# Kernel optimization log

Measured on AMD Instinct MI355X. Metric: run time of the kernel, lower is better.

Reference implementation:

```python
import jax, jax.numpy as jnp
import numpy as np

EPS = 1e-6

def setup_inputs() -> dict:
    key = jax.random.key(0)
    k1, k2, k3 = jax.random.split(key, 3)
    B, C, H, W = 2048, 256, 7, 7
    base = jax.random.normal(k1, (B, C, H, W), dtype=jnp.float32)
    moment = jax.random.normal(k2, (B, C, H, W), dtype=jnp.float32)
    A_matrix = jax.random.randint(k3, (B, H * W, H * W), 0, 2, dtype=jnp.int32)
    return {"base": base, "moment": moment, "A_matrix": A_matrix}

def reference(base, moment, A_matrix):
    B, C, H, W = base.shape
    P = H * W  # 49
    b = base.reshape(B, C, P)      # (B, C, 49)
    m = moment.reshape(B, C, P)    # (B, C, 49)
    # pairwise dot over channel dim via batched matmul (avoids BxCx49x49 broadcast)
    dots = jnp.einsum('bcp,bcq->bpq', b, m)            # (B, 49, 49)
    nb = jnp.maximum(jnp.linalg.norm(b, axis=1), EPS)  # (B, 49)
    nm = jnp.maximum(jnp.linalg.norm(m, axis=1), EPS)  # (B, 49)
    cos_sim = dots / (nb[:, :, None] * nm[:, None, :])
    mask = A_matrix.astype(bool)
    # masked mean without dynamic-size gather
    num = jnp.sum(jnp.where(mask, cos_sim, 0.0))
    den = jnp.sum(mask).astype(cos_sim.dtype)
    return -(num / den)
```

## Files before the change

### kernel.cpp

```cpp
#include <hip/hip_runtime.h>
#include <hip/hip_bf16.h>
#include <stdint.h>


typedef __attribute__((ext_vector_type(8))) short short8;
typedef __attribute__((ext_vector_type(4))) float floatx4;

#define P 49
#define CP 12544
#define NMASK 2401
#define MS_STRIDE 72

__device__ __forceinline__ short8 cvt8(float4 a, float4 b) {
  union { __hip_bfloat162 h2; short s2[2]; } t;
  short8 r;
  t.h2 = __float22bfloat162_rn(make_float2(a.x, a.y)); r[0] = t.s2[0]; r[1] = t.s2[1];
  t.h2 = __float22bfloat162_rn(make_float2(a.z, a.w)); r[2] = t.s2[0]; r[3] = t.s2[1];
  t.h2 = __float22bfloat162_rn(make_float2(b.x, b.y)); r[4] = t.s2[0]; r[5] = t.s2[1];
  t.h2 = __float22bfloat162_rn(make_float2(b.z, b.w)); r[6] = t.s2[0]; r[7] = t.s2[1];
  return r;
}

__global__ __launch_bounds__(512, 6) void pixpro_main(
    const float* __restrict__ base, const float* __restrict__ moment,
    const int* __restrict__ A, float* __restrict__ ws_num, float* __restrict__ ws_cnt)
{
  __shared__ __align__(16) uint16_t maskS[P * MS_STRIDE];
  __shared__ __align__(16) float normred[8 * 4 * 64];
  __shared__ __align__(16) float inv_nm_s[64];
  __shared__ __align__(16) float SQred[8 * 4 * 16 * 2];
  __shared__ float cntred[8];

  const int b    = blockIdx.x;
  const int tid  = threadIdx.x;
  const int lane = tid & 63;
  const int wv   = tid >> 6;
  const int mrow = lane & 15;
  const int kgrp = (lane >> 4) & 3;

  const float* gb = base   + (size_t)b * CP;
  const float* gm = moment + (size_t)b * CP;
  const int*   gA = A      + (size_t)b * NMASK;

  short8 afrag[2][2];
  float s0[8], s1[8];
  #pragma unroll
  for (int j = 0; j < 8; ++j) { s0[j] = 0.f; s1[j] = 0.f; }

  #pragma unroll
  for (int cti = 0; cti < 2; ++cti) {
    const int c = (2 * wv + cti) * 16 + mrow;
    const float* row = gm + c * P;
    float4 a0 = *(const float4*)(row + kgrp * 8);
    float4 a1 = *(const float4*)(row + kgrp * 8 + 4);
    float4 b0, b1;
    if (kgrp < 2) {
      b0 = *(const float4*)(row + 32 + kgrp * 8);
      b1 = *(const float4*)(row + 32 + kgrp * 8 + 4);
    } else if (kgrp == 2) {
      b0 = make_float4(row[48], 0.f, 0.f, 0.f);
      b1 = make_float4(0.f, 0.f, 0.f, 0.f);
    } else {
      b0 = make_float4(0.f, 0.f, 0.f, 0.f);
      b1 = make_float4(0.f, 0.f, 0.f, 0.f);
    }
    s0[0] = fmaf(a0.x, a0.x, s0[0]); s0[1] = fmaf(a0.y, a0.y, s0[1]);
    s0[2] = fmaf(a0.z, a0.z, s0[2]); s0[3] = fmaf(a0.w, a0.w, s0[3]);
    s0[4] = fmaf(a1.x, a1.x, s0[4]); s0[5] = fmaf(a1.y, a1.y, s0[5]);
    s0[6] = fmaf(a1.z, a1.z, s0[6]); s0[7] = fmaf(a1.w, a1.w, s0[7]);
    s1[0] = fmaf(b0.x, b0.x, s1[0]); s1[1] = fmaf(b0.y, b0.y, s1[1]);
    s1[2] = fmaf(b0.z, b0.z, s1[2]); s1[3] = fmaf(b0.w, b0.w, s1[3]);
    s1[4] = fmaf(b1.x, b1.x, s1[4]); s1[5] = fmaf(b1.y, b1.y, s1[5]);
    s1[6] = fmaf(b1.z, b1.z, s1[6]); s1[7] = fmaf(b1.w, b1.w, s1[7]);
    afrag[cti][0] = cvt8(a0, a1);
    afrag[cti][1] = cvt8(b0, b1);
  }

  const bool btask = tid < P * 8;
  const int  bp    = tid >> 3;
  const int  bqg   = tid & 7;
  const int  bq0   = bqg * 8;
  int bmask[8];
  #pragma unroll
  for (int j = 0; j < 8; ++j) bmask[j] = 0;
  if (btask) {
    const int* Ar = gA + bp * P + bq0;
    if (bqg <= 5) {
      int4 u0 = *(const int4*)(Ar);
      int4 u1 = *(const int4*)(Ar + 4);
      bmask[0] = u0.x; bmask[1] = u0.y; bmask[2] = u0.z; bmask[3] = u0.w;
      bmask[4] = u1.x; bmask[5] = u1.y; bmask[6] = u1.z; bmask[7] = u1.w;
    } else if (bqg == 6) {
      bmask[0] = Ar[0];
    }
  }

  #pragma unroll
  for (int j = 0; j < 8; ++j) {
    s0[j] += __shfl_xor(s0[j], 1); s0[j] += __shfl_xor(s0[j], 2);
    s1[j] += __shfl_xor(s1[j], 1); s1[j] += __shfl_xor(s1[j], 2);
  }
  if ((lane & 3) == 0) {
    const int h = mrow >> 2;
    float* nb_ = &normred[(wv * 4 + h) * 64 + kgrp * 8];
    *(float4*)(nb_ + 0)  = make_float4(s0[0], s0[1], s0[2], s0[3]);
    *(float4*)(nb_ + 4)  = make_float4(s0[4], s0[5], s0[6], s0[7]);
    *(float4*)(nb_ + 32) = make_float4(s1[0], s1[1], s1[2], s1[3]);
    *(float4*)(nb_ + 36) = make_float4(s1[4], s1[5], s1[6], s1[7]);
  }
  __syncthreads();

  if (tid < 64) {
    float s = 0.f;
    #pragma unroll
    for (int wh = 0; wh < 32; ++wh) s += normred[wh * 64 + tid];
    inv_nm_s[tid] = 1.0f / fmaxf(sqrtf(s), 1e-6f);
  }
  __syncthreads();

  int cntpart = 0;
  if (btask) {
    float4 i0 = *(const float4*)&inv_nm_s[bq0];
    float4 i1 = *(const float4*)&inv_nm_s[bq0 + 4];
    float4 f0, f1;
    f0.x = bmask[0] ? i0.x : 0.f; f0.y = bmask[1] ? i0.y : 0.f;
    f0.z = bmask[2] ? i0.z : 0.f; f0.w = bmask[3] ? i0.w : 0.f;
    f1.x = bmask[4] ? i1.x : 0.f; f1.y = bmask[5] ? i1.y : 0.f;
    f1.z = bmask[6] ? i1.z : 0.f; f1.w = bmask[7] ? i1.w : 0.f;
    #pragma unroll
    for (int j = 0; j < 8; ++j) cntpart += bmask[j];
    *(short8*)&maskS[bp * MS_STRIDE + bq0] = cvt8(f0, f1);
  }
  __syncthreads();

  const int pbase[4] = {0, 16, 32, 33};
  floatx4 acc[2][4];
  #pragma unroll
  for (int i = 0; i < 2; ++i)
    #pragma unroll
    for (int j = 0; j < 4; ++j) acc[i][j] = (floatx4){0.f, 0.f, 0.f, 0.f};

  #pragma unroll
  for (int kt = 0; kt < 2; ++kt) {
    short8 bfr[4];
    #pragma unroll
    for (int pt = 0; pt < 4; ++pt)
      bfr[pt] = *(const short8*)&maskS[(pbase[pt] + mrow) * MS_STRIDE + kt * 32 + kgrp * 8];
    #pragma unroll
    for (int cti = 0; cti < 2; ++cti)
      #pragma unroll
      for (int pt = 0; pt < 4; ++pt)
        acc[cti][pt] = __builtin_amdgcn_mfma_f32_16x16x32_bf16(afrag[cti][kt], bfr[pt], acc[cti][pt], 0, 0, 0);
  }

  float S[4] = {0.f, 0.f, 0.f, 0.f}, Qn[4] = {0.f, 0.f, 0.f, 0.f};
  #pragma unroll
  for (int cti = 0; cti < 2; ++cti) {
    float bv[4][4];
    #pragma unroll
    for (int pt = 0; pt < 4; ++pt) {
      const int pd = pbase[pt] + mrow;
      const bool pv = (pt < 3) || (mrow == 15);
      #pragma unroll
      for (int r = 0; r < 4; ++r) {
        const int c = (2 * wv + cti) * 16 + kgrp * 4 + r;
        float v = gb[c * P + pd];
        bv[pt][r] = pv ? v : 0.f;
      }
    }
    #pragma unroll
    for (int pt = 0; pt < 4; ++pt)
      #pragma unroll
      for (int r = 0; r < 4; ++r) {
        S[pt]  = fmaf(bv[pt][r], acc[cti][pt][r], S[pt]);
        Qn[pt] = fmaf(bv[pt][r], bv[pt][r], Qn[pt]);
      }
  }

  #pragma unroll
  for (int pt = 0; pt < 4; ++pt) {
    S[pt]  += __shfl_xor(S[pt], 16);  S[pt]  += __shfl_xor(S[pt], 32);
    Qn[pt] += __shfl_xor(Qn[pt], 16); Qn[pt] += __shfl_xor(Qn[pt], 32);
  }
  float cntf = (float)cntpart;
  #pragma unroll
  for (int off = 32; off > 0; off >>= 1) cntf += __shfl_xor(cntf, off);

  if (lane < 16) {
    #pragma unroll
    for (int pt = 0; pt < 4; ++pt)
      *(float2*)&SQred[((wv * 4 + pt) * 16 + mrow) * 2] = make_float2(S[pt], Qn[pt]);
  }
  if (lane == 0) cntred[wv] = cntf;
  __syncthreads();

  if (tid < 64) {
    float num = 0.f, cc = 0.f;
    if (tid < P) {
      const int pt = tid >> 4;
      const int mr = (pt == 3) ? 15 : (tid & 15);
      float Sp = 0.f, Qp = 0.f;
      #pragma unroll
      for (int w = 0; w < 8; ++w) {
        const int idx = ((w * 4 + pt) * 16 + mr) * 2;
        Sp += SQred[idx];
        Qp += SQred[idx + 1];
      }
      num = Sp * (1.0f / fmaxf(sqrtf(Qp), 1e-6f));
    }
    if (tid < 8) cc = cntred[tid];
    #pragma unroll
    for (int off = 32; off > 0; off >>= 1) {
      num += __shfl_xor(num, off);
      cc  += __shfl_xor(cc, off);
    }
    if (tid == 0) { ws_num[b] = num; ws_cnt[b] = cc; }
  }
}

__global__ __launch_bounds__(256) void pixpro_reduce(
    const float* __restrict__ ws_num, const float* __restrict__ ws_cnt,
    float* __restrict__ out)
{
  __shared__ float rn[4], rc[4];
  float n = 0.f, c = 0.f;
  for (int i = threadIdx.x; i < 2048; i += 256) { n += ws_num[i]; c += ws_cnt[i]; }
  #pragma unroll
  for (int off = 32; off > 0; off >>= 1) {
    n += __shfl_down(n, off, 64);
    c += __shfl_down(c, off, 64);
  }
  const int wv = threadIdx.x >> 6, lane = threadIdx.x & 63;
  if (lane == 0) { rn[wv] = n; rc[wv] = c; }
  __syncthreads();
  if (threadIdx.x == 0) {
    float N = rn[0] + rn[1] + rn[2] + rn[3];
    float D = rc[0] + rc[1] + rc[2] + rc[3];
    out[0] = -(N / D);
  }
}

extern "C" void kernel_launch(void* const* d_in, const int* in_sizes, int n_in,
                              void* d_out, int out_size, void* d_ws, size_t ws_size,
                              hipStream_t stream) {
  const float* base   = (const float*)d_in[0];
  const float* moment = (const float*)d_in[1];
  const int*   A      = (const int*)d_in[2];
  float* ws_num = (float*)d_ws;
  float* ws_cnt = ws_num + 2048;
  pixpro_main<<<2048, 512, 0, stream>>>(base, moment, A, ws_num, ws_cnt);
  pixpro_reduce<<<1, 256, 0, stream>>>(ws_num, ws_cnt, (float*)d_out);
}
```

Baseline: 235.3 us.

## Hoist base loads and norm computation before MFMA, drop final block barrier

The base tensor loads and their per-pixel squared norms now happen early, next to the moment loads, so their latency overlaps the mask and norm reductions instead of following the MFMA stage. The per-pixel inverse base norm is computed in shared memory before the matmul and folded into each wave's partial sum. Each wave writes its own partial numerator and count to the workspace, which removes the final block-level barrier and shared reduction. The cost is more live registers (launch bounds lowered from 6 to 4 waves per SIMD) and an 8x larger workspace for the reduce kernel to sum.

After: 239.6 us. About the same (+1.8%).

```diff
diff --git a/kernel.cpp b/kernel.cpp
--- a/kernel.cpp
+++ b/kernel.cpp
@@ -21,15 +21,15 @@
   return r;
 }
 
-__global__ __launch_bounds__(512, 6) void pixpro_main(
+__global__ __launch_bounds__(512, 4) void pixpro_main(
     const float* __restrict__ base, const float* __restrict__ moment,
     const int* __restrict__ A, float* __restrict__ ws_num, float* __restrict__ ws_cnt)
 {
   __shared__ __align__(16) uint16_t maskS[P * MS_STRIDE];
-  __shared__ __align__(16) float normred[8 * 4 * 64];
+  __shared__ __align__(16) float normred[32 * 64];
+  __shared__ __align__(16) float nbred[32 * 16];
   __shared__ __align__(16) float inv_nm_s[64];
-  __shared__ __align__(16) float SQred[8 * 4 * 16 * 2];
-  __shared__ float cntred[8];
+  __shared__ __align__(16) float inv_nb_s[64];
 
   const int b    = blockIdx.x;
   const int tid  = threadIdx.x;
@@ -42,11 +42,13 @@
   const float* gm = moment + (size_t)b * CP;
   const int*   gA = A      + (size_t)b * NMASK;
 
+  const int pbase[4] = {0, 16, 32, 33};
+
+
   short8 afrag[2][2];
   float s0[8], s1[8];
   #pragma unroll
   for (int j = 0; j < 8; ++j) { s0[j] = 0.f; s1[j] = 0.f; }
-
   #pragma unroll
   for (int cti = 0; cti < 2; ++cti) {
     const int c = (2 * wv + cti) * 16 + mrow;
@@ -95,6 +97,26 @@
     }
   }
 
+  float bv[2][4][4];
+  #pragma unroll
+  for (int cti = 0; cti < 2; ++cti)
+    #pragma unroll
+    for (int pt = 0; pt < 4; ++pt) {
+      const int pd = pbase[pt] + mrow;
+      #pragma unroll
+      for (int r = 0; r < 4; ++r) {
+        const int c = (2 * wv + cti) * 16 + kgrp * 4 + r;
+        bv[cti][pt][r] = gb[c * P + pd];
+      }
+    }
+  if (mrow != 15) {
+    #pragma unroll
+    for (int cti = 0; cti < 2; ++cti)
+      #pragma unroll
+      for (int r = 0; r < 4; ++r) bv[cti][3][r] = 0.f;
+  }
+
+
   #pragma unroll
   for (int j = 0; j < 8; ++j) {
     s0[j] += __shfl_xor(s0[j], 1); s0[j] += __shfl_xor(s0[j], 2);
@@ -108,6 +130,22 @@
     *(float4*)(nb_ + 32) = make_float4(s1[0], s1[1], s1[2], s1[3]);
     *(float4*)(nb_ + 36) = make_float4(s1[4], s1[5], s1[6], s1[7]);
   }
+
+  float sq[4];
+  #pragma unroll
+  for (int pt = 0; pt < 4; ++pt) {
+    float s = 0.f;
+    #pragma unroll
+    for (int cti = 0; cti < 2; ++cti)
+      #pragma unroll
+      for (int r = 0; r < 4; ++r) { float f = bv[cti][pt][r]; s = fmaf(f, f, s); }
+    s += __shfl_xor(s, 16); s += __shfl_xor(s, 32);
+    sq[pt] = s;
+  }
+  if (lane < 16) {
+    #pragma unroll
+    for (int pt = 0; pt < 4; ++pt) nbred[(wv * 4 + pt) * 16 + mrow] = sq[pt];
+  }
   __syncthreads();
 
   if (tid < 64) {
@@ -115,6 +153,16 @@
     #pragma unroll
     for (int wh = 0; wh < 32; ++wh) s += normred[wh * 64 + tid];
     inv_nm_s[tid] = 1.0f / fmaxf(sqrtf(s), 1e-6f);
+  } else if (tid < 128) {
+    const int p = tid - 64;
+    if (p < P) {
+      const int pt = (p == 48) ? 3 : (p >> 4);
+      const int mr = (p == 48) ? 15 : (p & 15);
+      float s = 0.f;
+      #pragma unroll
+      for (int w = 0; w < 8; ++w) s += nbred[(w * 4 + pt) * 16 + mr];
+      inv_nb_s[p] = 1.0f / fmaxf(sqrtf(s), 1e-6f);
+    }
   }
   __syncthreads();
 
@@ -131,15 +179,16 @@
     for (int j = 0; j < 8; ++j) cntpart += bmask[j];
     *(short8*)&maskS[bp * MS_STRIDE + bq0] = cvt8(f0, f1);
   }
-  __syncthreads();
-
-  const int pbase[4] = {0, 16, 32, 33};
+  float inb[4];
+  #pragma unroll
+  for (int pt = 0; pt < 4; ++pt) inb[pt] = inv_nb_s[pbase[pt] + mrow];
+  __syncthreads();
+
   floatx4 acc[2][4];
   #pragma unroll
   for (int i = 0; i < 2; ++i)
     #pragma unroll
     for (int j = 0; j < 4; ++j) acc[i][j] = (floatx4){0.f, 0.f, 0.f, 0.f};
-
   #pragma unroll
   for (int kt = 0; kt < 2; ++kt) {
     short8 bfr[4];
@@ -153,89 +202,48 @@
         acc[cti][pt] = __builtin_amdgcn_mfma_f32_16x16x32_bf16(afrag[cti][kt], bfr[pt], acc[cti][pt], 0, 0, 0);
   }
 
-  float S[4] = {0.f, 0.f, 0.f, 0.f}, Qn[4] = {0.f, 0.f, 0.f, 0.f};
-  #pragma unroll
-  for (int cti = 0; cti < 2; ++cti) {
-    float bv[4][4];
-    #pragma unroll
-    for (int pt = 0; pt < 4; ++pt) {
-      const int pd = pbase[pt] + mrow;
-      const bool pv = (pt < 3) || (mrow == 15);
-      #pragma unroll
-      for (int r = 0; r < 4; ++r) {
-        const int c = (2 * wv + cti) * 16 + kgrp * 4 + r;
-        float v = gb[c * P + pd];
-        bv[pt][r] = pv ? v : 0.f;
-      }
-    }
-    #pragma unroll
-    for (int pt = 0; pt < 4; ++pt)
-      #pragma unroll
-      for (int r = 0; r < 4; ++r) {
-        S[pt]  = fmaf(bv[pt][r], acc[cti][pt][r], S[pt]);
-        Qn[pt] = fmaf(bv[pt][r], bv[pt][r], Qn[pt]);
-      }
-  }
-
+  float num = 0.f;
   #pragma unroll
   for (int pt = 0; pt < 4; ++pt) {
-    S[pt]  += __shfl_xor(S[pt], 16);  S[pt]  += __shfl_xor(S[pt], 32);
-    Qn[pt] += __shfl_xor(Qn[pt], 16); Qn[pt] += __shfl_xor(Qn[pt], 32);
+    float tmp = 0.f;
+    #pragma unroll
+    for (int cti = 0; cti < 2; ++cti)
+      #pragma unroll
+      for (int r = 0; r < 4; ++r)
+        tmp = fmaf(bv[cti][pt][r], acc[cti][pt][r], tmp);
+    num = fmaf(inb[pt], tmp, num);
   }
   float cntf = (float)cntpart;
   #pragma unroll
-  for (int off = 32; off > 0; off >>= 1) cntf += __shfl_xor(cntf, off);
-
-  if (lane < 16) {
-    #pragma unroll
-    for (int pt = 0; pt < 4; ++pt)
-      *(float2*)&SQred[((wv * 4 + pt) * 16 + mrow) * 2] = make_float2(S[pt], Qn[pt]);
-  }
-  if (lane == 0) cntred[wv] = cntf;
-  __syncthreads();
-
-  if (tid < 64) {
-    float num = 0.f, cc = 0.f;
-    if (tid < P) {
-      const int pt = tid >> 4;
-      const int mr = (pt == 3) ? 15 : (tid & 15);
-      float Sp = 0.f, Qp = 0.f;
-      #pragma unroll
-      for (int w = 0; w < 8; ++w) {
-        const int idx = ((w * 4 + pt) * 16 + mr) * 2;
-        Sp += SQred[idx];
-        Qp += SQred[idx + 1];
-      }
-      num = Sp * (1.0f / fmaxf(sqrtf(Qp), 1e-6f));
-    }
-    if (tid < 8) cc = cntred[tid];
-    #pragma unroll
-    for (int off = 32; off > 0; off >>= 1) {
-      num += __shfl_xor(num, off);
-      cc  += __shfl_xor(cc, off);
-    }
-    if (tid == 0) { ws_num[b] = num; ws_cnt[b] = cc; }
-  }
-}
-
-__global__ __launch_bounds__(256) void pixpro_reduce(
+  for (int off = 32; off > 0; off >>= 1) {
+    num  += __shfl_xor(num, off);
+    cntf += __shfl_xor(cntf, off);
+  }
+  if (lane == 0) {
+    ws_num[b * 8 + wv] = num;
+    ws_cnt[b * 8 + wv] = cntf;
+  }
+}
+
+__global__ __launch_bounds__(512) void pixpro_reduce(
     const float* __restrict__ ws_num, const float* __restrict__ ws_cnt,
     float* __restrict__ out)
 {
-  __shared__ float rn[4], rc[4];
+  __shared__ float rn[8], rc[8];
   float n = 0.f, c = 0.f;
-  for (int i = threadIdx.x; i < 2048; i += 256) { n += ws_num[i]; c += ws_cnt[i]; }
+  for (int i = threadIdx.x; i < 16384; i += 512) { n += ws_num[i]; c += ws_cnt[i]; }
   #pragma unroll
   for (int off = 32; off > 0; off >>= 1) {
-    n += __shfl_down(n, off, 64);
-    c += __shfl_down(c, off, 64);
+    n += __shfl_xor(n, off);
+    c += __shfl_xor(c, off);
   }
   const int wv = threadIdx.x >> 6, lane = threadIdx.x & 63;
   if (lane == 0) { rn[wv] = n; rc[wv] = c; }
   __syncthreads();
   if (threadIdx.x == 0) {
-    float N = rn[0] + rn[1] + rn[2] + rn[3];
-    float D = rc[0] + rc[1] + rc[2] + rc[3];
+    float N = 0.f, D = 0.f;
+    #pragma unroll
+    for (int i = 0; i < 8; ++i) { N += rn[i]; D += rc[i]; }
     out[0] = -(N / D);
   }
 }
@@ -247,7 +255,7 @@
   const float* moment = (const float*)d_in[1];
   const int*   A      = (const int*)d_in[2];
   float* ws_num = (float*)d_ws;
-  float* ws_cnt = ws_num + 2048;
+  float* ws_cnt = ws_num + 16384;
   pixpro_main<<<2048, 512, 0, stream>>>(base, moment, A, ws_num, ws_cnt);
-  pixpro_reduce<<<1, 256, 0, stream>>>(ws_num, ws_cnt, (float*)d_out);
-}
+  pixpro_reduce<<<1, 512, 0, stream>>>(ws_num, ws_cnt, (float*)d_out);
+}
```
